# Kernel tuning notes

Measured on AMD Instinct MI355X. Metric: run time of the kernel, lower is better.

The kernel has to match this reference:

```python
import jax, jax.numpy as jnp
import numpy as np

B, L, D = 4, 2048, 1024
H, DH = 16, 64  # heads, head dim (D = H*DH)


def setup_inputs() -> dict:
    key = jax.random.key(0)
    k1, k2, k3 = jax.random.split(key, 3)
    scale = D ** -0.5
    xin = jax.random.normal(k1, (B, L, D), dtype=jnp.float32)
    W_qkv = jax.random.normal(k2, (D, 3 * D), dtype=jnp.float32) * scale
    W_o = jax.random.normal(k3, (D, D), dtype=jnp.float32) * scale
    return {"xin": xin, "W_qkv": W_qkv, "W_o": W_o}


def reference(xin, W_qkv, W_o):
    b, Lq, _ = xin.shape
    # QKV projection: (b, L, 3D). NOTE: original torch code reshapes the
    # (b, L, 3D) buffer directly to (b, 3, H, L, DH) — a non-standard axis
    # interleave — which we replicate faithfully.
    QKV = (xin @ W_qkv).reshape(b, 3, H, Lq, DH)
    Q, K, V = QKV[:, 0], QKV[:, 1], QKV[:, 2]  # each (b, H, L, DH)
    scores = jnp.einsum("bhqd,bhkd->bhqk", Q, K) * (DH ** -0.5)
    attn = jax.nn.softmax(scores, axis=-1)  # dropout_prob=0.0 -> identity
    out = jnp.einsum("bhqk,bhkd->bhqd", attn, V)
    out = out.transpose(0, 2, 1, 3).reshape(b, Lq, H * DH)
    return out @ W_o
```

## Files before the change

kernel.cpp:

```cpp
#include <hip/hip_runtime.h>
#include <stdint.h>

typedef short short8 __attribute__((ext_vector_type(8)));
typedef float f32x4 __attribute__((ext_vector_type(4)));

#define LOG2E 1.44269504088896f
#define AS1 __attribute__((address_space(1)))
#define AS3 __attribute__((address_space(3)))

__device__ __forceinline__ float fexp2(float x) {
#if __has_builtin(__builtin_amdgcn_exp2f)
    return __builtin_amdgcn_exp2f(x);
#else
    return exp2f(x);
#endif
}
__device__ __forceinline__ unsigned short f2bfbits(float f) {
    unsigned x = __builtin_bit_cast(unsigned, f);
    unsigned r = x + 0x7fffu + ((x >> 16) & 1u);
    return (unsigned short)(r >> 16);
}
__device__ __forceinline__ float bfbits2f(unsigned short b) {
    unsigned u = ((unsigned)b) << 16;
    return __builtin_bit_cast(float, u);
}
__device__ __forceinline__ void unpack8(uint4 u, float4& f0, float4& f1) {
    f0.x = bfbits2f((unsigned short)(u.x & 0xffffu)); f0.y = bfbits2f((unsigned short)(u.x >> 16));
    f0.z = bfbits2f((unsigned short)(u.y & 0xffffu)); f0.w = bfbits2f((unsigned short)(u.y >> 16));
    f1.x = bfbits2f((unsigned short)(u.z & 0xffffu)); f1.y = bfbits2f((unsigned short)(u.z >> 16));
    f1.z = bfbits2f((unsigned short)(u.w & 0xffffu)); f1.w = bfbits2f((unsigned short)(u.w >> 16));
}
__device__ __forceinline__ unsigned pack2(float a, float b) {
    return (unsigned)f2bfbits(a) | ((unsigned)f2bfbits(b) << 16);
}
__device__ __forceinline__ void glds16(const void* gp, void* lp) {
    __builtin_amdgcn_global_load_lds((const AS1 unsigned*)(uintptr_t)gp,
                                     (AS3 unsigned*)(unsigned)(uintptr_t)lp, 16, 0, 0);
}

__global__ __launch_bounds__(256) void xbf_k(const float* __restrict__ x,
                                             unsigned short* __restrict__ y) {
    int i = (blockIdx.x * 256 + threadIdx.x) * 4;
    float4 v = *(const float4*)(x + i);
    uint2 u;
    u.x = pack2(v.x, v.y);
    u.y = pack2(v.z, v.w);
    *(uint2*)(y + i) = u;
}

__global__ __launch_bounds__(256) void t32cvt_k(const float* __restrict__ src,
                                                unsigned short* __restrict__ dst,
                                                int R, int C) {
    __shared__ float tile[32][36];
    int t = threadIdx.x;
    int bx = blockIdx.x, by = blockIdx.y;
    int r = t >> 3, c0 = (t & 7) * 4;
    *(float4*)&tile[r][c0] = *(const float4*)(src + (size_t)(by * 32 + r) * C + bx * 32 + c0);
    __syncthreads();
    uint2 u;
    u.x = pack2(tile[c0 + 0][r], tile[c0 + 1][r]);
    u.y = pack2(tile[c0 + 2][r], tile[c0 + 3][r]);
    *(uint2*)(dst + (size_t)(bx * 32 + r) * R + by * 32 + c0) = u;
}

template <bool CF32>
__global__ __launch_bounds__(256) void gemm_k(const unsigned short* __restrict__ A,
                                              const unsigned short* __restrict__ Bt,
                                              void* __restrict__ Cv,
                                              int M, int N, int K) {
    __shared__ unsigned short sA[128 * 32];
    __shared__ unsigned short sB[128 * 32];
    int t = threadIdx.x;
    int wid = t >> 6, lane = t & 63;
    int wm = (wid >> 1) * 64, wn = (wid & 1) * 64;
    int lm = lane & 15, lq = lane >> 4;
    size_t m0 = (size_t)blockIdx.y * 128, n0 = (size_t)blockIdx.x * 128;
    int srow = t >> 2, scol = (t & 3) * 8;
    const unsigned short* ga0 = A + (m0 + srow) * K + scol;
    const unsigned short* ga1 = A + (m0 + 64 + srow) * K + scol;
    const unsigned short* gb0 = Bt + (n0 + srow) * K + scol;
    const unsigned short* gb1 = Bt + (n0 + 64 + srow) * K + scol;
    unsigned short* laA0 = &sA[wid * 512];
    unsigned short* laA1 = &sA[2048 + wid * 512];
    unsigned short* laB0 = &sB[wid * 512];
    unsigned short* laB1 = &sB[2048 + wid * 512];
    f32x4 acc[4][4] = {};
    for (int k0 = 0; k0 < K; k0 += 32) {
        __syncthreads();
        glds16(ga0 + k0, laA0);
        glds16(ga1 + k0, laA1);
        glds16(gb0 + k0, laB0);
        glds16(gb1 + k0, laB1);
        __syncthreads();
        short8 af[4], bfr[4];
        #pragma unroll
        for (int i = 0; i < 4; ++i) af[i] = *(const short8*)&sA[(wm + i * 16 + lm) * 32 + lq * 8];
        #pragma unroll
        for (int j = 0; j < 4; ++j) bfr[j] = *(const short8*)&sB[(wn + j * 16 + lm) * 32 + lq * 8];
        #pragma unroll
        for (int i = 0; i < 4; ++i)
            #pragma unroll
            for (int j = 0; j < 4; ++j)
                acc[i][j] = __builtin_amdgcn_mfma_f32_16x16x32_bf16(af[i], bfr[j], acc[i][j], 0, 0, 0);
    }
    #pragma unroll
    for (int i = 0; i < 4; ++i)
        #pragma unroll
        for (int j = 0; j < 4; ++j)
            #pragma unroll
            for (int r = 0; r < 4; ++r) {
                size_t row = m0 + wm + i * 16 + lq * 4 + r;
                size_t col = n0 + wn + j * 16 + lm;
                if (CF32) ((float*)Cv)[row * N + col] = acc[i][j][r];
                else ((unsigned short*)Cv)[row * N + col] = f2bfbits(acc[i][j][r]);
            }
}

__global__ __launch_bounds__(256) void vt_k(const unsigned short* __restrict__ qkv,
                                            unsigned short* __restrict__ vt) {
    __shared__ unsigned short tile[64 * 72];
    int kt = blockIdx.x, bh = blockIdx.y;
    int b = bh >> 4, h = bh & 15;
    const unsigned short* Vp = qkv + (size_t)b * 6291456 + 4194304 + (size_t)h * 131072;
    int t = threadIdx.x;
    int row = t >> 2, cc = (t & 3) * 16;
    const unsigned short* src = Vp + (size_t)(kt * 64 + row) * 64 + cc;
    *(uint4*)&tile[row * 72 + cc] = *(const uint4*)src;
    *(uint4*)&tile[row * 72 + cc + 8] = *(const uint4*)(src + 8);
    __syncthreads();
    unsigned v[8];
    #pragma unroll
    for (int j = 0; j < 8; ++j) {
        unsigned short a = tile[(cc + 2 * j) * 72 + row];
        unsigned short bsh = tile[(cc + 2 * j + 1) * 72 + row];
        v[j] = (unsigned)a | ((unsigned)bsh << 16);
    }
    unsigned short* dst = vt + ((size_t)bh * 64 + row) * 2048 + kt * 64 + cc;
    *(uint4*)dst = make_uint4(v[0], v[1], v[2], v[3]);
    *(uint4*)(dst + 8) = make_uint4(v[4], v[5], v[6], v[7]);
}

__global__ __launch_bounds__(256, 2) void attn_mfma(const unsigned short* __restrict__ qkv,
                                                    const unsigned short* __restrict__ vt,
                                                    unsigned short* __restrict__ aout) {
    __shared__ unsigned short Ks[64 * 72];
    __shared__ unsigned short Vs[64 * 72];
    __shared__ unsigned short Ps[4 * 64 * 72];
    int bid = blockIdx.x;
    int qt = bid & 7, h = (bid >> 3) & 15, b = bid >> 7;
    int t = threadIdx.x;
    int wave = t >> 6, lane = t & 63, lm = lane & 15, quad = lane >> 4;
    const unsigned short* Qb = qkv + (size_t)b * 6291456 + (size_t)h * 131072;
    const unsigned short* Kb = Qb + 2097152;
    const unsigned short* Vtb = vt + (size_t)(b * 16 + h) * 131072;
    int q0 = qt * 256 + wave * 64;

    const float qs = 0.125f * LOG2E;
    short8 qf[4][2];
    #pragma unroll
    for (int i = 0; i < 4; ++i)
        #pragma unroll
        for (int c = 0; c < 2; ++c) {
            uint4 u = *(const uint4*)(Qb + (size_t)(q0 + i * 16 + lm) * 64 + c * 32 + quad * 8);
            float4 f0, f1; unpack8(u, f0, f1);
            uint4 v;
            v.x = pack2(f0.x * qs, f0.y * qs);
            v.y = pack2(f0.z * qs, f0.w * qs);
            v.z = pack2(f1.x * qs, f1.y * qs);
            v.w = pack2(f1.z * qs, f1.w * qs);
            qf[i][c] = *(short8*)&v;
        }

    short8 ones;
    #pragma unroll
    for (int z = 0; z < 8; ++z) ones[z] = (short)0x3F80;

    f32x4 o[4][4] = {};
    f32x4 l_acc[4] = {};

    int srow = t >> 2, scol = (t & 3) * 16;
    unsigned short* psw = Ps + wave * 4608;

    for (int kt = 0; kt < 32; ++kt) {
        const unsigned short* kp = Kb + (size_t)(kt * 64 + srow) * 64 + scol;
        uint4 k0 = *(const uint4*)kp;
        uint4 k1 = *(const uint4*)(kp + 8);
        const unsigned short* vp = Vtb + (size_t)srow * 2048 + kt * 64 + scol;
        uint4 v0 = *(const uint4*)vp;
        uint4 v1 = *(const uint4*)(vp + 8);
        __syncthreads();
        *(uint4*)&Ks[srow * 72 + scol] = k0;
        *(uint4*)&Ks[srow * 72 + scol + 8] = k1;
        *(uint4*)&Vs[srow * 72 + scol] = v0;
        *(uint4*)&Vs[srow * 72 + scol + 8] = v1;
        __syncthreads();

        #pragma unroll
        for (int j = 0; j < 4; ++j) {
            short8 kf0 = *(const short8*)&Ks[(j * 16 + lm) * 72 + quad * 8];
            short8 kf1 = *(const short8*)&Ks[(j * 16 + lm) * 72 + 32 + quad * 8];
            f32x4 sf[4];
            #pragma unroll
            for (int i = 0; i < 4; ++i) {
                sf[i] = (f32x4){0.f, 0.f, 0.f, 0.f};
                sf[i] = __builtin_amdgcn_mfma_f32_16x16x32_bf16(qf[i][0], kf0, sf[i], 0, 0, 0);
                sf[i] = __builtin_amdgcn_mfma_f32_16x16x32_bf16(qf[i][1], kf1, sf[i], 0, 0, 0);
            }
            #pragma unroll
            for (int i = 0; i < 4; ++i)
                #pragma unroll
                for (int r = 0; r < 4; ++r) {
                    float p = fexp2(sf[i][r]);
                    unsigned bits = __builtin_bit_cast(unsigned, p);
                    psw[(i * 16 + quad * 4 + r) * 72 + j * 16 + lm] = (unsigned short)(bits >> 16);
                }
        }
        __syncthreads();

        #pragma unroll
        for (int c = 0; c < 2; ++c) {
            short8 pf[4];
            #pragma unroll
            for (int i = 0; i < 4; ++i)
                pf[i] = *(const short8*)&psw[(i * 16 + lm) * 72 + c * 32 + quad * 8];
            #pragma unroll
            for (int jd = 0; jd < 4; ++jd) {
                short8 vf = *(const short8*)&Vs[(jd * 16 + lm) * 72 + c * 32 + quad * 8];
                #pragma unroll
                for (int i = 0; i < 4; ++i)
                    o[i][jd] = __builtin_amdgcn_mfma_f32_16x16x32_bf16(pf[i], vf, o[i][jd], 0, 0, 0);
            }
            #pragma unroll
            for (int i = 0; i < 4; ++i)
                l_acc[i] = __builtin_amdgcn_mfma_f32_16x16x32_bf16(pf[i], ones, l_acc[i], 0, 0, 0);
        }
    }
    #pragma unroll
    for (int i = 0; i < 4; ++i)
        #pragma unroll
        for (int r = 0; r < 4; ++r) {
            float inv = 1.f / l_acc[i][r];
            int q = q0 + i * 16 + quad * 4 + r;
            size_t rowbase = ((size_t)b * 2048 + q) * 1024 + h * 64;
            #pragma unroll
            for (int jd = 0; jd < 4; ++jd)
                aout[rowbase + jd * 16 + lm] = f2bfbits(o[i][jd][r] * inv);
        }
}

extern "C" void kernel_launch(void* const* d_in, const int* in_sizes, int n_in,
                              void* d_out, int out_size, void* d_ws, size_t ws_size,
                              hipStream_t stream) {
    const float* xin  = (const float*)d_in[0];
    const float* wqkv = (const float*)d_in[1];
    const float* wo   = (const float*)d_in[2];
    float* out = (float*)d_out;

    char* ws = (char*)d_ws;
    unsigned short* qkv   = (unsigned short*)(ws);
    unsigned short* attn  = (unsigned short*)(ws + 50331648);
    unsigned short* wqkvT = (unsigned short*)(ws + 67108864);
    unsigned short* woT   = (unsigned short*)(ws + 73400320);
    unsigned short* vt    = (unsigned short*)(ws + 75497472);
    unsigned short* xb    = (unsigned short*)(ws + 92274688);

    dim3 blk(256);
    xbf_k<<<dim3(8192), blk, 0, stream>>>(xin, xb);
    t32cvt_k<<<dim3(3072 / 32, 1024 / 32), blk, 0, stream>>>(wqkv, wqkvT, 1024, 3072);
    t32cvt_k<<<dim3(1024 / 32, 1024 / 32), blk, 0, stream>>>(wo, woT, 1024, 1024);
    gemm_k<false><<<dim3(3072 / 128, 8192 / 128), blk, 0, stream>>>(xb, wqkvT, qkv, 8192, 3072, 1024);
    vt_k<<<dim3(32, 64), blk, 0, stream>>>(qkv, vt);
    attn_mfma<<<dim3(512), blk, 0, stream>>>(qkv, vt, attn);
    gemm_k<true><<<dim3(1024 / 128, 8192 / 128), blk, 0, stream>>>(attn, woT, out, 8192, 1024, 1024);
}
```

Before: 292.9 us.

## Shrink attention query tile, prefetch K/V in registers, transpose score MFMA

```diff
diff --git a/kernel.cpp b/kernel.cpp
--- a/kernel.cpp
+++ b/kernel.cpp
@@ -32,6 +32,11 @@
 }
 __device__ __forceinline__ unsigned pack2(float a, float b) {
     return (unsigned)f2bfbits(a) | ((unsigned)f2bfbits(b) << 16);
+}
+__device__ __forceinline__ unsigned pack2t(float a, float b) {
+    unsigned ba = __builtin_bit_cast(unsigned, a);
+    unsigned bb = __builtin_bit_cast(unsigned, b);
+    return (ba >> 16) | (bb & 0xffff0000u);
 }
 __device__ __forceinline__ void glds16(const void* gp, void* lp) {
     __builtin_amdgcn_global_load_lds((const AS1 unsigned*)(uintptr_t)gp,
@@ -140,25 +145,25 @@
     *(uint4*)(dst + 8) = make_uint4(v[4], v[5], v[6], v[7]);
 }
 
-__global__ __launch_bounds__(256, 2) void attn_mfma(const unsigned short* __restrict__ qkv,
+__global__ __launch_bounds__(256, 4) void attn_mfma(const unsigned short* __restrict__ qkv,
                                                     const unsigned short* __restrict__ vt,
                                                     unsigned short* __restrict__ aout) {
     __shared__ unsigned short Ks[64 * 72];
     __shared__ unsigned short Vs[64 * 72];
-    __shared__ unsigned short Ps[4 * 64 * 72];
+    __shared__ unsigned short Ps[4 * 32 * 72];
     int bid = blockIdx.x;
-    int qt = bid & 7, h = (bid >> 3) & 15, b = bid >> 7;
+    int qt = bid & 15, h = (bid >> 4) & 15, b = bid >> 8;
     int t = threadIdx.x;
     int wave = t >> 6, lane = t & 63, lm = lane & 15, quad = lane >> 4;
     const unsigned short* Qb = qkv + (size_t)b * 6291456 + (size_t)h * 131072;
     const unsigned short* Kb = Qb + 2097152;
     const unsigned short* Vtb = vt + (size_t)(b * 16 + h) * 131072;
-    int q0 = qt * 256 + wave * 64;
+    int q0 = qt * 128 + wave * 32;
 
     const float qs = 0.125f * LOG2E;
-    short8 qf[4][2];
-    #pragma unroll
-    for (int i = 0; i < 4; ++i)
+    short8 qf[2][2];
+    #pragma unroll
+    for (int i = 0; i < 2; ++i)
         #pragma unroll
         for (int c = 0; c < 2; ++c) {
             uint4 u = *(const uint4*)(Qb + (size_t)(q0 + i * 16 + lm) * 64 + c * 32 + quad * 8);
@@ -175,68 +180,76 @@
     #pragma unroll
     for (int z = 0; z < 8; ++z) ones[z] = (short)0x3F80;
 
-    f32x4 o[4][4] = {};
-    f32x4 l_acc[4] = {};
+    f32x4 o[2][4] = {};
+    f32x4 l_acc[2] = {};
 
     int srow = t >> 2, scol = (t & 3) * 16;
-    unsigned short* psw = Ps + wave * 4608;
-
+    unsigned short* psw = Ps + wave * (32 * 72);
+
+    uint4 k0r, k1r, v0r, v1r;
+    {
+        const unsigned short* kp = Kb + (size_t)srow * 64 + scol;
+        k0r = *(const uint4*)kp;
+        k1r = *(const uint4*)(kp + 8);
+        const unsigned short* vp = Vtb + (size_t)srow * 2048 + scol;
+        v0r = *(const uint4*)vp;
+        v1r = *(const uint4*)(vp + 8);
+    }
+
+    #pragma unroll 1
     for (int kt = 0; kt < 32; ++kt) {
-        const unsigned short* kp = Kb + (size_t)(kt * 64 + srow) * 64 + scol;
-        uint4 k0 = *(const uint4*)kp;
-        uint4 k1 = *(const uint4*)(kp + 8);
-        const unsigned short* vp = Vtb + (size_t)srow * 2048 + kt * 64 + scol;
-        uint4 v0 = *(const uint4*)vp;
-        uint4 v1 = *(const uint4*)(vp + 8);
-        __syncthreads();
-        *(uint4*)&Ks[srow * 72 + scol] = k0;
-        *(uint4*)&Ks[srow * 72 + scol + 8] = k1;
-        *(uint4*)&Vs[srow * 72 + scol] = v0;
-        *(uint4*)&Vs[srow * 72 + scol + 8] = v1;
-        __syncthreads();
+        __syncthreads();
+        *(uint4*)&Ks[srow * 72 + scol] = k0r;
+        *(uint4*)&Ks[srow * 72 + scol + 8] = k1r;
+        *(uint4*)&Vs[srow * 72 + scol] = v0r;
+        *(uint4*)&Vs[srow * 72 + scol + 8] = v1r;
+        __syncthreads();
+
+        if (kt < 31) {
+            const unsigned short* kp = Kb + (size_t)((kt + 1) * 64 + srow) * 64 + scol;
+            k0r = *(const uint4*)kp;
+            k1r = *(const uint4*)(kp + 8);
+            const unsigned short* vp = Vtb + (size_t)srow * 2048 + (kt + 1) * 64 + scol;
+            v0r = *(const uint4*)vp;
+            v1r = *(const uint4*)(vp + 8);
+        }
 
         #pragma unroll
         for (int j = 0; j < 4; ++j) {
             short8 kf0 = *(const short8*)&Ks[(j * 16 + lm) * 72 + quad * 8];
             short8 kf1 = *(const short8*)&Ks[(j * 16 + lm) * 72 + 32 + quad * 8];
-            f32x4 sf[4];
-            #pragma unroll
-            for (int i = 0; i < 4; ++i) {
-                sf[i] = (f32x4){0.f, 0.f, 0.f, 0.f};
-                sf[i] = __builtin_amdgcn_mfma_f32_16x16x32_bf16(qf[i][0], kf0, sf[i], 0, 0, 0);
-                sf[i] = __builtin_amdgcn_mfma_f32_16x16x32_bf16(qf[i][1], kf1, sf[i], 0, 0, 0);
+            #pragma unroll
+            for (int i = 0; i < 2; ++i) {
+                f32x4 sf = {0.f, 0.f, 0.f, 0.f};
+                sf = __builtin_amdgcn_mfma_f32_16x16x32_bf16(kf0, qf[i][0], sf, 0, 0, 0);
+                sf = __builtin_amdgcn_mfma_f32_16x16x32_bf16(kf1, qf[i][1], sf, 0, 0, 0);
+                uint2 u;
+                u.x = pack2t(fexp2(sf[0]), fexp2(sf[1]));
+                u.y = pack2t(fexp2(sf[2]), fexp2(sf[3]));
+                *(uint2*)&psw[(i * 16 + lm) * 72 + j * 16 + quad * 4] = u;
             }
-            #pragma unroll
-            for (int i = 0; i < 4; ++i)
-                #pragma unroll
-                for (int r = 0; r < 4; ++r) {
-                    float p = fexp2(sf[i][r]);
-                    unsigned bits = __builtin_bit_cast(unsigned, p);
-                    psw[(i * 16 + quad * 4 + r) * 72 + j * 16 + lm] = (unsigned short)(bits >> 16);
-                }
-        }
-        __syncthreads();
+        }
 
         #pragma unroll
         for (int c = 0; c < 2; ++c) {
-            short8 pf[4];
-            #pragma unroll
-            for (int i = 0; i < 4; ++i)
+            short8 pf[2];
+            #pragma unroll
+            for (int i = 0; i < 2; ++i)
                 pf[i] = *(const short8*)&psw[(i * 16 + lm) * 72 + c * 32 + quad * 8];
             #pragma unroll
             for (int jd = 0; jd < 4; ++jd) {
                 short8 vf = *(const short8*)&Vs[(jd * 16 + lm) * 72 + c * 32 + quad * 8];
                 #pragma unroll
-                for (int i = 0; i < 4; ++i)
+                for (int i = 0; i < 2; ++i)
                     o[i][jd] = __builtin_amdgcn_mfma_f32_16x16x32_bf16(pf[i], vf, o[i][jd], 0, 0, 0);
             }
             #pragma unroll
-            for (int i = 0; i < 4; ++i)
+            for (int i = 0; i < 2; ++i)
                 l_acc[i] = __builtin_amdgcn_mfma_f32_16x16x32_bf16(pf[i], ones, l_acc[i], 0, 0, 0);
         }
     }
     #pragma unroll
-    for (int i = 0; i < 4; ++i)
+    for (int i = 0; i < 2; ++i)
         #pragma unroll
         for (int r = 0; r < 4; ++r) {
             float inv = 1.f / l_acc[i][r];
@@ -270,6 +283,6 @@
     t32cvt_k<<<dim3(1024 / 32, 1024 / 32), blk, 0, stream>>>(wo, woT, 1024, 1024);
     gemm_k<false><<<dim3(3072 / 128, 8192 / 128), blk, 0, stream>>>(xb, wqkvT, qkv, 8192, 3072, 1024);
     vt_k<<<dim3(32, 64), blk, 0, stream>>>(qkv, vt);
-    attn_mfma<<<dim3(512), blk, 0, stream>>>(qkv, vt, attn);
+    attn_mfma<<<dim3(1024), blk, 0, stream>>>(qkv, vt, attn);
     gemm_k<true><<<dim3(1024 / 128, 8192 / 128), blk, 0, stream>>>(attn, woT, out, 8192, 1024, 1024);
 }
```

New measurement: 300.2 us. 1.03x slower.
